# Performance work log

Measured on AMD Instinct MI355X. Metric: run time of the kernel, lower is better.

Reference implementation:

```python
import jax, jax.numpy as jnp
import numpy as np

TAU = 2.0      # spikingjelly LIFNode default tau
V_TH = 1.0     # default v_threshold
ALPHA = 4.0    # default surrogate.Sigmoid alpha


@jax.custom_vjp
def spike_fn(v):
    # Heaviside(v - v_th) with sigmoid surrogate gradient
    return (v >= V_TH).astype(v.dtype)

def _spike_fwd(v):
    return (v >= V_TH).astype(v.dtype), v

def _spike_bwd(v, g):
    s = jax.nn.sigmoid(ALPHA * (v - V_TH))
    return (g * ALPHA * s * (1.0 - s),)

spike_fn.defvjp(_spike_fwd, _spike_bwd)


def lif(x):
    """Multi-step LIF: decay_input=False, hard reset to v_reset=0, detach_reset.
    x: [T, B, C, N] -> spikes [T, B, C, N]."""
    def step(v, xt):
        v = v * (1.0 - 1.0 / TAU) + xt          # v = v - (v - 0)/tau + x
        s = spike_fn(v)
        v = v * (1.0 - jax.lax.stop_gradient(s))  # hard reset, detached spike
        return v, s
    v0 = jnp.zeros_like(x[0])
    _, spikes = jax.lax.scan(step, v0, x)
    return spikes


def setup_inputs() -> dict:
    key = jax.random.key(0)
    kx, k1, k2, k3 = jax.random.split(key, 4)
    T, B, C, dim = 4, 32, 196, 768
    scale = dim ** -0.5
    x = jax.random.normal(kx, (T, B, C, dim), dtype=jnp.float32)
    w1 = jax.random.normal(k1, (dim, dim), dtype=jnp.float32) * scale
    w2 = jax.random.normal(k2, (dim, dim), dtype=jnp.float32) * scale
    w3 = jax.random.normal(k3, (dim, dim), dtype=jnp.float32) * scale
    return {"x": x, "w1": w1, "w2": w2, "w3": w3}


def reference(x, w1, w2, w3):
    # y1 = mlp1(mlp1_lif(x)); y2 = mlp2(mlp2_lif(x)); out = mlp3(y1 * mlp3_lif(y2))
    y1 = jnp.einsum('tbcn,mn->tbcm', lif(x), w1)
    y2 = jnp.einsum('tbcn,mn->tbcm', lif(x), w2)
    out = jnp.einsum('tbcn,mn->tbcm', y1 * lif(y2), w3)
    return out
```

## Files before the change

kernel.cpp:

```cpp
#include <hip/hip_runtime.h>
#include <stdint.h>

#define T_STEPS 4
#define BC      6272
#define NDIM    768
#define TBC     (T_STEPS*BC)
#define BCN     (BC*NDIM)
#define FIX_CAP 65536

typedef unsigned short u16;
typedef __attribute__((ext_vector_type(8))) __bf16 bf16x8;
typedef __attribute__((ext_vector_type(4))) float f32x4;
typedef __attribute__((ext_vector_type(4))) int   i32x4;

#define MFMA16(a,b,c)  __builtin_amdgcn_mfma_f32_16x16x32_bf16((a),(b),(c),0,0,0)
#define MFMAI8(a,b,c)  __builtin_amdgcn_mfma_i32_16x16x64_i8((a),(b),(c),0,0,0)

__device__ __forceinline__ u16 f2b(float f) {
    uint32_t u = __builtin_bit_cast(uint32_t, f);
    u += 0x7FFFu + ((u >> 16) & 1u);
    return (u16)(u >> 16);
}
__device__ __forceinline__ void gload16(const void* g, void* l) {
    __builtin_amdgcn_global_load_lds((const __attribute__((address_space(1))) void*)g,
                                     (__attribute__((address_space(3))) void*)l,
                                     16, 0, 0);
}

__global__ __launch_bounds__(256) void lif_x_kernel(const float* __restrict__ x,
                                                    int8_t* __restrict__ s8) {
    int gid = blockIdx.x * 256 + threadIdx.x;
    double v0 = 0, v1 = 0, v2 = 0, v3 = 0;
    #pragma unroll
    for (int t = 0; t < T_STEPS; ++t) {
        float4 xv = *(const float4*)&x[(size_t)t * BCN + (size_t)gid * 4];
        uint32_t pack = 0;
        v0 = 0.5 * v0 + (double)xv.x; if (v0 >= 1.0) { pack |= 1u;       v0 = 0.0; }
        v1 = 0.5 * v1 + (double)xv.y; if (v1 >= 1.0) { pack |= 1u << 8;  v1 = 0.0; }
        v2 = 0.5 * v2 + (double)xv.z; if (v2 >= 1.0) { pack |= 1u << 16; v2 = 0.0; }
        v3 = 0.5 * v3 + (double)xv.w; if (v3 >= 1.0) { pack |= 1u << 24; v3 = 0.0; }
        *(uint32_t*)&s8[(size_t)t * BCN + (size_t)gid * 4] = pack;
    }
}

__global__ __launch_bounds__(256) void cnt_kernel(const int8_t* __restrict__ s8,
                                                  u16* __restrict__ cnt) {
    int row  = blockIdx.x * 4 + (threadIdx.x >> 6);
    int lane = threadIdx.x & 63;
    const uint32_t* p = (const uint32_t*)(s8 + (size_t)row * NDIM + lane * 12);
    uint32_t sum = 0;
    #pragma unroll
    for (int j = 0; j < 3; ++j) sum += (p[j] * 0x01010101u) >> 24;
    #pragma unroll
    for (int o = 32; o > 0; o >>= 1) sum += __shfl_xor(sum, o);
    if (lane == 0) cnt[row] = (u16)sum;
}

__global__ __launch_bounds__(256) void prep_w_kernel(
    const float* __restrict__ w1, const float* __restrict__ w2,
    const float* __restrict__ w3,
    int8_t* __restrict__ w1q, int8_t* __restrict__ w2h,
    int8_t* __restrict__ w2l, u16* __restrict__ w3b,
    uint32_t* __restrict__ fix_cnt) {
    int i = blockIdx.x * 256 + threadIdx.x;
    if (i == 0) *fix_cnt = 0;
    int q1 = __float2int_rn(w1[i] * 512.0f);
    q1 = q1 > 127 ? 127 : (q1 < -127 ? -127 : q1);
    w1q[i] = (int8_t)q1;
    int q16 = __double2int_rn((double)w2[i] * 65536.0);
    int8_t lo = (int8_t)(q16 & 0xFF);
    int hi = (q16 - (int)lo) >> 8;
    w2h[i] = (int8_t)hi;
    w2l[i] = lo;
    w3b[i] = f2b(w3[i]);
}

__global__ __launch_bounds__(256) void y12_kernel(
    const int8_t* __restrict__ s8,
    const int8_t* __restrict__ w1q, const int8_t* __restrict__ w2hb,
    const int8_t* __restrict__ w2lb,
    const u16* __restrict__ cnt,
    u16* __restrict__ z,
    uint32_t* __restrict__ fix_cnt,
    int2* __restrict__ fix_idx, float4* __restrict__ fix_y1)
{
    __shared__ int8_t lds[2][40960];

    const int tid  = threadIdx.x;
    const int lane = tid & 63;
    const int wid  = tid >> 6;

    const int bid = blockIdx.x;
    const int swz = (bid & 7) * 294 + (bid >> 3);
    const int mb  = swz % (NDIM / 64);
    const int rb  = swz / (NDIM / 64);
    const int m0  = mb * 64;
    const int bc0 = rb * 32;

    const int srow  = lane >> 3;
    const int scolB = ((lane & 7) << 4) ^ (srow << 4);
    const int8_t* gp[10];
    int lofs[10];
    #pragma unroll
    for (int c = 0; c < 10; ++c) {
        int chunk = wid * 10 + c;
        const int8_t* g;
        int l;
        if (chunk < 16) {
            int gr = chunk * 8 + srow;
            int t = gr >> 5, bcl = gr & 31;
            g = s8 + ((size_t)(t * BC + bc0 + bcl)) * NDIM + scolB;
            l = chunk * 1024;
        } else if (chunk < 24) {
            int mr = (chunk - 16) * 8 + srow;
            g = w1q + ((size_t)(m0 + mr)) * NDIM + scolB;
            l = 16384 + (chunk - 16) * 1024;
        } else if (chunk < 32) {
            int mr = (chunk - 24) * 8 + srow;
            g = w2hb + ((size_t)(m0 + mr)) * NDIM + scolB;
            l = 24576 + (chunk - 24) * 1024;
        } else {
            int mr = (chunk - 32) * 8 + srow;
            g = w2lb + ((size_t)(m0 + mr)) * NDIM + scolB;
            l = 32768 + (chunk - 32) * 1024;
        }
        gp[c] = g;
        lofs[c] = l;
    }

    const int key = lane & 7;
    const int g4  = lane >> 4;
    int slotA[2];
    slotA[0] = ((g4     ^ key) << 4);
    slotA[1] = (((4|g4) ^ key) << 4);
    int abase[8];
    #pragma unroll
    for (int t = 0; t < 4; ++t)
        #pragma unroll
        for (int rt = 0; rt < 2; ++rt)
            abase[t * 2 + rt] = (t * 32 + rt * 16 + (lane & 15)) * 128;
    const int bbase = (wid * 16 + (lane & 15)) * 128;

    i32x4 acc1[4][2], acch[4][2], accl[4][2];
    #pragma unroll
    for (int t = 0; t < 4; ++t)
        #pragma unroll
        for (int rt = 0; rt < 2; ++rt) {
            acc1[t][rt] = (i32x4){0, 0, 0, 0};
            acch[t][rt] = (i32x4){0, 0, 0, 0};
            accl[t][rt] = (i32x4){0, 0, 0, 0};
        }

    auto stage = [&](int buf) {
        #pragma unroll
        for (int c = 0; c < 10; ++c) {
            gload16(gp[c], &lds[buf][lofs[c]]);
            gp[c] += 128;
        }
    };
    auto compute = [&](int buf) {
        const int8_t* L = lds[buf];
        #pragma unroll
        for (int ks = 0; ks < 2; ++ks) {
            const int sl = slotA[ks];
            i32x4 b1 = *(const i32x4*)&L[16384 + bbase + sl];
            i32x4 bh = *(const i32x4*)&L[24576 + bbase + sl];
            i32x4 bl = *(const i32x4*)&L[32768 + bbase + sl];
            #pragma unroll
            for (int t = 0; t < 4; ++t)
                #pragma unroll
                for (int rt = 0; rt < 2; ++rt) {
                    i32x4 a = *(const i32x4*)&L[abase[t * 2 + rt] + sl];
                    acc1[t][rt] = MFMAI8(a, b1, acc1[t][rt]);
                    acch[t][rt] = MFMAI8(a, bh, acch[t][rt]);
                    accl[t][rt] = MFMAI8(a, bl, accl[t][rt]);
                }
        }
    };

    stage(0);
    __syncthreads();
    #pragma unroll
    for (int it = 0; it < 5; ++it) {
        stage((it + 1) & 1);
        compute(it & 1);
        __syncthreads();
    }
    compute(1);

    const int mg = m0 + wid * 16 + (lane & 15);
    #pragma unroll
    for (int rt = 0; rt < 2; ++rt) {
        #pragma unroll
        for (int r = 0; r < 4; ++r) {
            const int bcg = bc0 + rt * 16 + (lane >> 4) * 4 + r;
            double v = 0.0, e = 0.0;
            bool flag = false;
            float zv[4], y1v[4];
            #pragma unroll
            for (int t = 0; t < 4; ++t) {
                float y1 = (float)acc1[t][rt][r] * (1.0f / 512.0f);
                y1v[t] = y1;
                double y2 = (double)(acch[t][rt][r] * 256 + accl[t][rt][r])
                            * (1.0 / 65536.0);
                v = 0.5 * v + y2;
                e = 0.5 * e + 7.62939453125e-6 * (double)cnt[t * BC + bcg] + 1e-9;
                double d = v - 1.0;
                flag |= (d <= e && d >= -e);
                if (v >= 1.0) { zv[t] = y1; v = 0.0; }
                else          { zv[t] = 0.0f; }
            }
            if (flag) {
                uint32_t id = atomicAdd(fix_cnt, 1u);
                if (id < FIX_CAP) {
                    fix_idx[id] = make_int2(bcg, mg);
                    fix_y1[id]  = make_float4(y1v[0], y1v[1], y1v[2], y1v[3]);
                }
            }
            #pragma unroll
            for (int t = 0; t < 4; ++t)
                z[((size_t)(t * BC + bcg)) * NDIM + mg] = f2b(zv[t]);
        }
    }
}

__global__ __launch_bounds__(256) void fixup_kernel(
    const int8_t* __restrict__ s8, const float* __restrict__ w2,
    const int2* __restrict__ fix_idx, const float4* __restrict__ fix_y1,
    const uint32_t* __restrict__ fix_cnt, u16* __restrict__ z)
{
    const int lane = threadIdx.x & 63;
    const int wave = (blockIdx.x * 256 + threadIdx.x) >> 6;
    const int nw   = gridDim.x * 4;
    uint32_t n = *fix_cnt;
    if (n > FIX_CAP) n = FIX_CAP;

    for (uint32_t e = wave; e < n; e += nw) {
        const int bc = fix_idx[e].x, m = fix_idx[e].y;
        const float* w2row = w2 + (size_t)m * NDIM;
        double acc[4] = {0.0, 0.0, 0.0, 0.0};
        #pragma unroll
        for (int j = 0; j < NDIM / 64; ++j) {
            int nn = lane + j * 64;
            double wv = (double)w2row[nn];
            #pragma unroll
            for (int t = 0; t < 4; ++t)
                if (s8[((size_t)(t * BC + bc)) * NDIM + nn]) acc[t] += wv;
        }
        #pragma unroll
        for (int o = 32; o > 0; o >>= 1)
            #pragma unroll
            for (int t = 0; t < 4; ++t) acc[t] += __shfl_xor(acc[t], o);
        if (lane == 0) {
            float4 y1 = fix_y1[e];
            float y1a[4] = {y1.x, y1.y, y1.z, y1.w};
            double v = 0.0;
            #pragma unroll
            for (int t = 0; t < 4; ++t) {
                v = 0.5 * v + acc[t];
                u16 zz = 0;
                if (v >= 1.0) { zz = f2b(y1a[t]); v = 0.0; }
                z[((size_t)(t * BC + bc)) * NDIM + m] = zz;
            }
        }
    }
}

__global__ __launch_bounds__(256) void out_kernel(
    const u16* __restrict__ z, const u16* __restrict__ w3b,
    float* __restrict__ out)
{
    __shared__ u16 lds[2][8192];

    const int tid  = threadIdx.x;
    const int lane = tid & 63;
    const int wid  = tid >> 6;

    const int bid = blockIdx.x;
    const int swz = (bid & 7) * 588 + (bid >> 3);
    const int mb  = swz % (NDIM / 64);
    const int rb  = swz / (NDIM / 64);
    const int m0  = mb * 64;
    const int r0  = rb * 64;

    const int lrow  = lane >> 3;
    const int scolE = ((((lane & 7) << 4) ^ (lrow << 4)) >> 1);
    const u16* gp[4];
    int lofs[4];
    #pragma unroll
    for (int c = 0; c < 4; ++c) {
        int chunk = wid * 4 + c;
        const u16* g;
        if (chunk < 8) {
            int grow = chunk * 8 + lrow;
            g = z + ((size_t)(r0 + grow)) * NDIM + scolE;
        } else {
            int grow = (chunk - 8) * 8 + lrow;
            g = w3b + ((size_t)(m0 + grow)) * NDIM + scolE;
        }
        gp[c] = g;
        lofs[c] = chunk * 512;
    }

    const int swzb = (lane & 7) << 4;
    const int cb   = (lane >> 4) << 4;
    const int colE0 = ((cb     ) ^ swzb) >> 1;
    const int colE1 = ((cb | 64) ^ swzb) >> 1;
    const int boff = (wid * 16 + (lane & 15)) * 64;

    f32x4 acc[4];
    #pragma unroll
    for (int rt = 0; rt < 4; ++rt) acc[rt] = (f32x4){0.f, 0.f, 0.f, 0.f};

    auto stage = [&](int buf) {
        #pragma unroll
        for (int c = 0; c < 4; ++c) {
            gload16(gp[c], &lds[buf][lofs[c]]);
            gp[c] += 64;
        }
    };
    auto compute = [&](int buf) {
        const u16* L = lds[buf];
        #pragma unroll
        for (int k2i = 0; k2i < 2; ++k2i) {
            const int ce = k2i ? colE1 : colE0;
            bf16x8 bw = *(const bf16x8*)&L[4096 + boff + ce];
            #pragma unroll
            for (int rt = 0; rt < 4; ++rt) {
                bf16x8 az = *(const bf16x8*)&L[(rt * 16 + (lane & 15)) * 64 + ce];
                acc[rt] = MFMA16(az, bw, acc[rt]);
            }
        }
    };

    stage(0);
    __syncthreads();
    for (int it = 0; it < 11; ++it) {
        stage((it + 1) & 1);
        compute(it & 1);
        __syncthreads();
    }
    compute(1);

    #pragma unroll
    for (int rt = 0; rt < 4; ++rt)
        #pragma unroll
        for (int r = 0; r < 4; ++r)
            out[((size_t)(r0 + rt * 16 + (lane >> 4) * 4 + r)) * NDIM
                + m0 + wid * 16 + (lane & 15)] = acc[rt][r];
}

extern "C" void kernel_launch(void* const* d_in, const int* in_sizes, int n_in,
                              void* d_out, int out_size, void* d_ws, size_t ws_size,
                              hipStream_t stream) {
    const float* x  = (const float*)d_in[0];
    const float* w1 = (const float*)d_in[1];
    const float* w2 = (const float*)d_in[2];
    const float* w3 = (const float*)d_in[3];
    float* out = (float*)d_out;

    char* ws = (char*)d_ws;
    int8_t*   s8      = (int8_t*)(ws);
    u16*      z       = (u16*)(ws + 19267584);
    int8_t*   w1q     = (int8_t*)(ws + 57802752);
    int8_t*   w2h     = (int8_t*)(ws + 58392576);
    int8_t*   w2l     = (int8_t*)(ws + 58982400);
    u16*      w3b     = (u16*)(ws + 59572224);
    u16*      cnt     = (u16*)(ws + 60751872);
    uint32_t* fix_cnt = (uint32_t*)(ws + 60802048);
    int2*     fix_idx = (int2*)(ws + 60802112);
    float4*   fix_y1  = (float4*)(ws + 61326400);

    prep_w_kernel<<<(NDIM * NDIM) / 256, 256, 0, stream>>>(w1, w2, w3, w1q, w2h,
                                                           w2l, w3b, fix_cnt);
    lif_x_kernel<<<BCN / 4 / 256, 256, 0, stream>>>(x, s8);
    cnt_kernel<<<TBC / 4, 256, 0, stream>>>(s8, cnt);
    y12_kernel<<<(BC / 32) * (NDIM / 64), 256, 0, stream>>>(s8, w1q, w2h, w2l,
                                                            cnt, z, fix_cnt,
                                                            fix_idx, fix_y1);
    fixup_kernel<<<128, 256, 0, stream>>>(s8, w2, fix_idx, fix_y1, fix_cnt, z);
    out_kernel<<<(TBC / 64) * (NDIM / 64), 256, 0, stream>>>(z, w3b, out);
}
```

Before: 146.7 us.

## Fuse LIF with spike counting and enlarge GEMM tiles in y12 and out kernels

Merges the LIF spike kernel and the per-row count kernel into one pass, so the spike buffer is not re-read to get counts. The y12 GEMM tile grows from 64 to 128 output columns with a K step of 64, and the out GEMM tile grows from 64x64 to 128x128 with a 2x2 warp layout. Both GEMMs gain occupancy hints. Larger tiles raise data reuse per LDS load, at the cost of more accumulator registers and fewer blocks. It also resets the error bound after a spike in the near-threshold check.

```diff
diff --git a/kernel.cpp b/kernel.cpp
--- a/kernel.cpp
+++ b/kernel.cpp
@@ -27,33 +27,52 @@
                                      16, 0, 0);
 }
 
-__global__ __launch_bounds__(256) void lif_x_kernel(const float* __restrict__ x,
-                                                    int8_t* __restrict__ s8) {
-    int gid = blockIdx.x * 256 + threadIdx.x;
-    double v0 = 0, v1 = 0, v2 = 0, v3 = 0;
+__global__ __launch_bounds__(256) void lifcnt_kernel(const float* __restrict__ x,
+                                                     int8_t* __restrict__ s8,
+                                                     u16* __restrict__ cnt) {
+    const int bc   = blockIdx.x * 4 + (threadIdx.x >> 6);
+    const int lane = threadIdx.x & 63;
+    const size_t base = (size_t)bc * NDIM + lane * 12;
+
+    double v[12];
+    #pragma unroll
+    for (int j = 0; j < 12; ++j) v[j] = 0.0;
+    uint32_t c01 = 0, c23 = 0;
+
     #pragma unroll
     for (int t = 0; t < T_STEPS; ++t) {
-        float4 xv = *(const float4*)&x[(size_t)t * BCN + (size_t)gid * 4];
-        uint32_t pack = 0;
-        v0 = 0.5 * v0 + (double)xv.x; if (v0 >= 1.0) { pack |= 1u;       v0 = 0.0; }
-        v1 = 0.5 * v1 + (double)xv.y; if (v1 >= 1.0) { pack |= 1u << 8;  v1 = 0.0; }
-        v2 = 0.5 * v2 + (double)xv.z; if (v2 >= 1.0) { pack |= 1u << 16; v2 = 0.0; }
-        v3 = 0.5 * v3 + (double)xv.w; if (v3 >= 1.0) { pack |= 1u << 24; v3 = 0.0; }
-        *(uint32_t*)&s8[(size_t)t * BCN + (size_t)gid * 4] = pack;
-    }
-}
-
-__global__ __launch_bounds__(256) void cnt_kernel(const int8_t* __restrict__ s8,
-                                                  u16* __restrict__ cnt) {
-    int row  = blockIdx.x * 4 + (threadIdx.x >> 6);
-    int lane = threadIdx.x & 63;
-    const uint32_t* p = (const uint32_t*)(s8 + (size_t)row * NDIM + lane * 12);
-    uint32_t sum = 0;
-    #pragma unroll
-    for (int j = 0; j < 3; ++j) sum += (p[j] * 0x01010101u) >> 24;
-    #pragma unroll
-    for (int o = 32; o > 0; o >>= 1) sum += __shfl_xor(sum, o);
-    if (lane == 0) cnt[row] = (u16)sum;
+        float4 xa = *(const float4*)&x[(size_t)t * BCN + base + 0];
+        float4 xb = *(const float4*)&x[(size_t)t * BCN + base + 4];
+        float4 xc = *(const float4*)&x[(size_t)t * BCN + base + 8];
+        float xs[12] = {xa.x, xa.y, xa.z, xa.w, xb.x, xb.y, xb.z, xb.w,
+                        xc.x, xc.y, xc.z, xc.w};
+        uint32_t pk[3] = {0, 0, 0};
+        uint32_t csum = 0;
+        #pragma unroll
+        for (int j = 0; j < 12; ++j) {
+            v[j] = 0.5 * v[j] + (double)xs[j];
+            if (v[j] >= 1.0) {
+                pk[j >> 2] |= 1u << ((j & 3) * 8);
+                csum++;
+                v[j] = 0.0;
+            }
+        }
+        uint32_t* dst = (uint32_t*)&s8[(size_t)t * BCN + base];
+        dst[0] = pk[0]; dst[1] = pk[1]; dst[2] = pk[2];
+        if (t < 2) c01 += csum << (t * 16);
+        else       c23 += csum << ((t - 2) * 16);
+    }
+    #pragma unroll
+    for (int o = 32; o > 0; o >>= 1) {
+        c01 += __shfl_xor(c01, o);
+        c23 += __shfl_xor(c23, o);
+    }
+    if (lane == 0) {
+        cnt[0 * BC + bc] = (u16)(c01 & 0xFFFF);
+        cnt[1 * BC + bc] = (u16)(c01 >> 16);
+        cnt[2 * BC + bc] = (u16)(c23 & 0xFFFF);
+        cnt[3 * BC + bc] = (u16)(c23 >> 16);
+    }
 }
 
 __global__ __launch_bounds__(256) void prep_w_kernel(
@@ -75,7 +94,7 @@
     w3b[i] = f2b(w3[i]);
 }
 
-__global__ __launch_bounds__(256) void y12_kernel(
+__global__ __launch_bounds__(256, 2) void y12_kernel(
     const int8_t* __restrict__ s8,
     const int8_t* __restrict__ w1q, const int8_t* __restrict__ w2hb,
     const int8_t* __restrict__ w2lb,
@@ -84,144 +103,149 @@
     uint32_t* __restrict__ fix_cnt,
     int2* __restrict__ fix_idx, float4* __restrict__ fix_y1)
 {
-    __shared__ int8_t lds[2][40960];
+    __shared__ int8_t lds[2][32768];
 
     const int tid  = threadIdx.x;
     const int lane = tid & 63;
     const int wid  = tid >> 6;
 
     const int bid = blockIdx.x;
-    const int swz = (bid & 7) * 294 + (bid >> 3);
-    const int mb  = swz % (NDIM / 64);
-    const int rb  = swz / (NDIM / 64);
-    const int m0  = mb * 64;
+    const int swz = (bid & 7) * 147 + (bid >> 3);
+    const int mb  = swz % (NDIM / 128);
+    const int rb  = swz / (NDIM / 128);
+    const int m0  = mb * 128;
     const int bc0 = rb * 32;
 
-    const int srow  = lane >> 3;
-    const int scolB = ((lane & 7) << 4) ^ (srow << 4);
-    const int8_t* gp[10];
-    int lofs[10];
-    #pragma unroll
-    for (int c = 0; c < 10; ++c) {
-        int chunk = wid * 10 + c;
+    const int srow  = lane >> 2;
+    const int scolB = ((lane & 3) ^ (srow & 3)) << 4;
+    const int8_t* gp[8];
+    int lofs[8];
+    #pragma unroll
+    for (int c = 0; c < 8; ++c) {
+        int chunk = wid * 8 + c;
         const int8_t* g;
         int l;
-        if (chunk < 16) {
-            int gr = chunk * 8 + srow;
+        if (chunk < 8) {
+            int gr = chunk * 16 + srow;
             int t = gr >> 5, bcl = gr & 31;
             g = s8 + ((size_t)(t * BC + bc0 + bcl)) * NDIM + scolB;
             l = chunk * 1024;
+        } else if (chunk < 16) {
+            int mr = (chunk - 8) * 16 + srow;
+            g = w1q + ((size_t)(m0 + mr)) * NDIM + scolB;
+            l = 8192 + (chunk - 8) * 1024;
         } else if (chunk < 24) {
-            int mr = (chunk - 16) * 8 + srow;
-            g = w1q + ((size_t)(m0 + mr)) * NDIM + scolB;
+            int mr = (chunk - 16) * 16 + srow;
+            g = w2hb + ((size_t)(m0 + mr)) * NDIM + scolB;
             l = 16384 + (chunk - 16) * 1024;
-        } else if (chunk < 32) {
-            int mr = (chunk - 24) * 8 + srow;
-            g = w2hb + ((size_t)(m0 + mr)) * NDIM + scolB;
+        } else {
+            int mr = (chunk - 24) * 16 + srow;
+            g = w2lb + ((size_t)(m0 + mr)) * NDIM + scolB;
             l = 24576 + (chunk - 24) * 1024;
-        } else {
-            int mr = (chunk - 32) * 8 + srow;
-            g = w2lb + ((size_t)(m0 + mr)) * NDIM + scolB;
-            l = 32768 + (chunk - 32) * 1024;
         }
         gp[c] = g;
         lofs[c] = l;
     }
 
-    const int key = lane & 7;
-    const int g4  = lane >> 4;
-    int slotA[2];
-    slotA[0] = ((g4     ^ key) << 4);
-    slotA[1] = (((4|g4) ^ key) << 4);
-    int abase[8];
+    const int soff = (((lane >> 4) ^ (lane & 3)) << 4);
+    int aoff[4][2];
     #pragma unroll
     for (int t = 0; t < 4; ++t)
         #pragma unroll
         for (int rt = 0; rt < 2; ++rt)
-            abase[t * 2 + rt] = (t * 32 + rt * 16 + (lane & 15)) * 128;
-    const int bbase = (wid * 16 + (lane & 15)) * 128;
-
-    i32x4 acc1[4][2], acch[4][2], accl[4][2];
+            aoff[t][rt] = (t * 32 + rt * 16 + (lane & 15)) * 64 + soff;
+    int boff[2];
+    #pragma unroll
+    for (int mf = 0; mf < 2; ++mf)
+        boff[mf] = (wid * 32 + mf * 16 + (lane & 15)) * 64 + soff;
+
+    i32x4 a1[4][2][2], ah[4][2][2], al[4][2][2];
     #pragma unroll
     for (int t = 0; t < 4; ++t)
         #pragma unroll
-        for (int rt = 0; rt < 2; ++rt) {
-            acc1[t][rt] = (i32x4){0, 0, 0, 0};
-            acch[t][rt] = (i32x4){0, 0, 0, 0};
-            accl[t][rt] = (i32x4){0, 0, 0, 0};
-        }
+        for (int rt = 0; rt < 2; ++rt)
+            #pragma unroll
+            for (int mf = 0; mf < 2; ++mf) {
+                a1[t][rt][mf] = (i32x4){0, 0, 0, 0};
+                ah[t][rt][mf] = (i32x4){0, 0, 0, 0};
+                al[t][rt][mf] = (i32x4){0, 0, 0, 0};
+            }
 
     auto stage = [&](int buf) {
         #pragma unroll
-        for (int c = 0; c < 10; ++c) {
+        for (int c = 0; c < 8; ++c) {
             gload16(gp[c], &lds[buf][lofs[c]]);
-            gp[c] += 128;
+            gp[c] += 64;
         }
     };
     auto compute = [&](int buf) {
         const int8_t* L = lds[buf];
-        #pragma unroll
-        for (int ks = 0; ks < 2; ++ks) {
-            const int sl = slotA[ks];
-            i32x4 b1 = *(const i32x4*)&L[16384 + bbase + sl];
-            i32x4 bh = *(const i32x4*)&L[24576 + bbase + sl];
-            i32x4 bl = *(const i32x4*)&L[32768 + bbase + sl];
-            #pragma unroll
-            for (int t = 0; t < 4; ++t)
+        i32x4 b1[2], bh[2], bl[2];
+        #pragma unroll
+        for (int mf = 0; mf < 2; ++mf) {
+            b1[mf] = *(const i32x4*)&L[ 8192 + boff[mf]];
+            bh[mf] = *(const i32x4*)&L[16384 + boff[mf]];
+            bl[mf] = *(const i32x4*)&L[24576 + boff[mf]];
+        }
+        #pragma unroll
+        for (int t = 0; t < 4; ++t)
+            #pragma unroll
+            for (int rt = 0; rt < 2; ++rt) {
+                i32x4 a = *(const i32x4*)&L[aoff[t][rt]];
                 #pragma unroll
-                for (int rt = 0; rt < 2; ++rt) {
-                    i32x4 a = *(const i32x4*)&L[abase[t * 2 + rt] + sl];
-                    acc1[t][rt] = MFMAI8(a, b1, acc1[t][rt]);
-                    acch[t][rt] = MFMAI8(a, bh, acch[t][rt]);
-                    accl[t][rt] = MFMAI8(a, bl, accl[t][rt]);
+                for (int mf = 0; mf < 2; ++mf) {
+                    a1[t][rt][mf] = MFMAI8(a, b1[mf], a1[t][rt][mf]);
+                    ah[t][rt][mf] = MFMAI8(a, bh[mf], ah[t][rt][mf]);
+                    al[t][rt][mf] = MFMAI8(a, bl[mf], al[t][rt][mf]);
                 }
-        }
+            }
     };
 
     stage(0);
     __syncthreads();
-    #pragma unroll
-    for (int it = 0; it < 5; ++it) {
+    for (int it = 0; it < 11; ++it) {
         stage((it + 1) & 1);
         compute(it & 1);
         __syncthreads();
     }
     compute(1);
 
-    const int mg = m0 + wid * 16 + (lane & 15);
-    #pragma unroll
-    for (int rt = 0; rt < 2; ++rt) {
-        #pragma unroll
-        for (int r = 0; r < 4; ++r) {
-            const int bcg = bc0 + rt * 16 + (lane >> 4) * 4 + r;
-            double v = 0.0, e = 0.0;
-            bool flag = false;
-            float zv[4], y1v[4];
-            #pragma unroll
-            for (int t = 0; t < 4; ++t) {
-                float y1 = (float)acc1[t][rt][r] * (1.0f / 512.0f);
-                y1v[t] = y1;
-                double y2 = (double)(acch[t][rt][r] * 256 + accl[t][rt][r])
-                            * (1.0 / 65536.0);
-                v = 0.5 * v + y2;
-                e = 0.5 * e + 7.62939453125e-6 * (double)cnt[t * BC + bcg] + 1e-9;
-                double d = v - 1.0;
-                flag |= (d <= e && d >= -e);
-                if (v >= 1.0) { zv[t] = y1; v = 0.0; }
-                else          { zv[t] = 0.0f; }
-            }
-            if (flag) {
-                uint32_t id = atomicAdd(fix_cnt, 1u);
-                if (id < FIX_CAP) {
-                    fix_idx[id] = make_int2(bcg, mg);
-                    fix_y1[id]  = make_float4(y1v[0], y1v[1], y1v[2], y1v[3]);
+    #pragma unroll
+    for (int rt = 0; rt < 2; ++rt)
+        #pragma unroll
+        for (int mf = 0; mf < 2; ++mf) {
+            const int mg = m0 + wid * 32 + mf * 16 + (lane & 15);
+            #pragma unroll
+            for (int r = 0; r < 4; ++r) {
+                const int bcg = bc0 + rt * 16 + (lane >> 4) * 4 + r;
+                double v = 0.0, e = 0.0;
+                bool flag = false;
+                float zv[4], y1v[4];
+                #pragma unroll
+                for (int t = 0; t < 4; ++t) {
+                    float y1 = (float)a1[t][rt][mf][r] * (1.0f / 512.0f);
+                    y1v[t] = y1;
+                    double y2 = (double)(ah[t][rt][mf][r] * 256 + al[t][rt][mf][r])
+                                * (1.0 / 65536.0);
+                    v = 0.5 * v + y2;
+                    e = 0.5 * e + 7.62939453125e-6 * (double)cnt[t * BC + bcg] + 1e-9;
+                    double d = v - 1.0;
+                    flag |= (d <= e && d >= -e);
+                    if (v >= 1.0) { zv[t] = y1; v = 0.0; e = 0.0; }
+                    else          { zv[t] = 0.0f; }
                 }
-            }
-            #pragma unroll
-            for (int t = 0; t < 4; ++t)
-                z[((size_t)(t * BC + bcg)) * NDIM + mg] = f2b(zv[t]);
-        }
-    }
+                if (flag) {
+                    uint32_t id = atomicAdd(fix_cnt, 1u);
+                    if (id < FIX_CAP) {
+                        fix_idx[id] = make_int2(bcg, mg);
+                        fix_y1[id]  = make_float4(y1v[0], y1v[1], y1v[2], y1v[3]);
+                    }
+                }
+                #pragma unroll
+                for (int t = 0; t < 4; ++t)
+                    z[((size_t)(t * BC + bcg)) * NDIM + mg] = f2b(zv[t]);
+            }
+        }
 }
 
 __global__ __launch_bounds__(256) void fixup_kernel(
@@ -266,37 +290,39 @@
     }
 }
 
-__global__ __launch_bounds__(256) void out_kernel(
+__global__ __launch_bounds__(256, 2) void out_kernel(
     const u16* __restrict__ z, const u16* __restrict__ w3b,
     float* __restrict__ out)
 {
-    __shared__ u16 lds[2][8192];
+    __shared__ u16 lds[2][16384];
 
     const int tid  = threadIdx.x;
     const int lane = tid & 63;
     const int wid  = tid >> 6;
+    const int rw   = wid >> 1;
+    const int cw   = wid & 1;
 
     const int bid = blockIdx.x;
-    const int swz = (bid & 7) * 588 + (bid >> 3);
-    const int mb  = swz % (NDIM / 64);
-    const int rb  = swz / (NDIM / 64);
-    const int m0  = mb * 64;
-    const int r0  = rb * 64;
-
-    const int lrow  = lane >> 3;
-    const int scolE = ((((lane & 7) << 4) ^ (lrow << 4)) >> 1);
-    const u16* gp[4];
-    int lofs[4];
-    #pragma unroll
-    for (int c = 0; c < 4; ++c) {
-        int chunk = wid * 4 + c;
+    const int swz = (bid & 7) * 147 + (bid >> 3);
+    const int mb  = swz % (NDIM / 128);
+    const int rb  = swz / (NDIM / 128);
+    const int m0  = mb * 128;
+    const int r0  = rb * 128;
+
+    const int srow  = lane >> 3;
+    const int scolE = ((((lane & 7) << 4) ^ ((srow & 7) << 4)) >> 1);
+    const u16* gp[8];
+    int lofs[8];
+    #pragma unroll
+    for (int c = 0; c < 8; ++c) {
+        int chunk = wid * 8 + c;
         const u16* g;
-        if (chunk < 8) {
-            int grow = chunk * 8 + lrow;
-            g = z + ((size_t)(r0 + grow)) * NDIM + scolE;
+        if (chunk < 16) {
+            int gr = chunk * 8 + srow;
+            g = z + ((size_t)(r0 + gr)) * NDIM + scolE;
         } else {
-            int grow = (chunk - 8) * 8 + lrow;
-            g = w3b + ((size_t)(m0 + grow)) * NDIM + scolE;
+            int mr = (chunk - 16) * 8 + srow;
+            g = w3b + ((size_t)(m0 + mr)) * NDIM + scolE;
         }
         gp[c] = g;
         lofs[c] = chunk * 512;
@@ -306,15 +332,16 @@
     const int cb   = (lane >> 4) << 4;
     const int colE0 = ((cb     ) ^ swzb) >> 1;
     const int colE1 = ((cb | 64) ^ swzb) >> 1;
-    const int boff = (wid * 16 + (lane & 15)) * 64;
-
-    f32x4 acc[4];
-    #pragma unroll
-    for (int rt = 0; rt < 4; ++rt) acc[rt] = (f32x4){0.f, 0.f, 0.f, 0.f};
+
+    f32x4 acc[4][4];
+    #pragma unroll
+    for (int rt = 0; rt < 4; ++rt)
+        #pragma unroll
+        for (int cf = 0; cf < 4; ++cf) acc[rt][cf] = (f32x4){0.f, 0.f, 0.f, 0.f};
 
     auto stage = [&](int buf) {
         #pragma unroll
-        for (int c = 0; c < 4; ++c) {
+        for (int c = 0; c < 8; ++c) {
             gload16(gp[c], &lds[buf][lofs[c]]);
             gp[c] += 64;
         }
@@ -324,11 +351,16 @@
         #pragma unroll
         for (int k2i = 0; k2i < 2; ++k2i) {
             const int ce = k2i ? colE1 : colE0;
-            bf16x8 bw = *(const bf16x8*)&L[4096 + boff + ce];
+            bf16x8 bw[4];
+            #pragma unroll
+            for (int cf = 0; cf < 4; ++cf)
+                bw[cf] = *(const bf16x8*)&L[8192 + (cw * 64 + cf * 16 + (lane & 15)) * 64 + ce];
             #pragma unroll
             for (int rt = 0; rt < 4; ++rt) {
-                bf16x8 az = *(const bf16x8*)&L[(rt * 16 + (lane & 15)) * 64 + ce];
-                acc[rt] = MFMA16(az, bw, acc[rt]);
+                bf16x8 az = *(const bf16x8*)&L[(rw * 64 + rt * 16 + (lane & 15)) * 64 + ce];
+                #pragma unroll
+                for (int cf = 0; cf < 4; ++cf)
+                    acc[rt][cf] = MFMA16(az, bw[cf], acc[rt][cf]);
             }
         }
     };
@@ -345,9 +377,11 @@
     #pragma unroll
     for (int rt = 0; rt < 4; ++rt)
         #pragma unroll
-        for (int r = 0; r < 4; ++r)
-            out[((size_t)(r0 + rt * 16 + (lane >> 4) * 4 + r)) * NDIM
-                + m0 + wid * 16 + (lane & 15)] = acc[rt][r];
+        for (int cf = 0; cf < 4; ++cf)
+            #pragma unroll
+            for (int r = 0; r < 4; ++r)
+                out[((size_t)(r0 + rw * 64 + rt * 16 + (lane >> 4) * 4 + r)) * NDIM
+                    + m0 + cw * 64 + cf * 16 + (lane & 15)] = acc[rt][cf][r];
 }
 
 extern "C" void kernel_launch(void* const* d_in, const int* in_sizes, int n_in,
@@ -373,11 +407,10 @@
 
     prep_w_kernel<<<(NDIM * NDIM) / 256, 256, 0, stream>>>(w1, w2, w3, w1q, w2h,
                                                            w2l, w3b, fix_cnt);
-    lif_x_kernel<<<BCN / 4 / 256, 256, 0, stream>>>(x, s8);
-    cnt_kernel<<<TBC / 4, 256, 0, stream>>>(s8, cnt);
-    y12_kernel<<<(BC / 32) * (NDIM / 64), 256, 0, stream>>>(s8, w1q, w2h, w2l,
-                                                            cnt, z, fix_cnt,
-                                                            fix_idx, fix_y1);
+    lifcnt_kernel<<<BC / 4, 256, 0, stream>>>(x, s8, cnt);
+    y12_kernel<<<(BC / 32) * (NDIM / 128), 256, 0, stream>>>(s8, w1q, w2h, w2l,
+                                                             cnt, z, fix_cnt,
+                                                             fix_idx, fix_y1);
     fixup_kernel<<<128, 256, 0, stream>>>(s8, w2, fix_idx, fix_y1, fix_cnt, z);
-    out_kernel<<<(TBC / 64) * (NDIM / 64), 256, 0, stream>>>(z, w3b, out);
-}
+    out_kernel<<<(TBC / 128) * (NDIM / 128), 256, 0, stream>>>(z, w3b, out);
+}
```

New measurement: 167.5 us. 1.14x slower.
